# Kernel optimization log

Measured on AMD Instinct MI355X. Metric: run time of the kernel, lower is better.

## Reference

```python
import jax, jax.numpy as jnp
import numpy as np

B, L, R, D, K, H = 512, 10, 2048, 256, 20, 128
VOCAB, GEO_V, GEO_D = 30000, 1000, 64

def _l2norm(x):
    # F.normalize(p=2, dim=-1): x / max(||x||, eps)
    return x / jnp.maximum(jnp.linalg.norm(x, axis=-1, keepdims=True), 1e-12)

def setup_inputs() -> dict:
    key = jax.random.key(0)
    ks = jax.random.split(key, 20)
    emb = 0.02 * jax.random.normal(ks[0], (VOCAB, D), jnp.float32)
    emb = emb.at[0].set(0.0)  # padding_idx=0 row is zero
    inp = {
        'text_left': jax.random.randint(ks[1], (B, L), 0, VOCAB),
        'text_right': jax.random.randint(ks[2], (B, R), 0, VOCAB),
        'location_left': jax.random.randint(ks[3], (B, 2), 0, GEO_V),
        'distance': jax.random.uniform(ks[4], (B,), jnp.float32),
        'emb': emb,
        'attn_w': 0.05 * jax.random.normal(ks[5], (D,), jnp.float32),
        'w_m0': 0.1 * jax.random.normal(ks[6], (K, H), jnp.float32),
        'b_m0': jnp.zeros((H,), jnp.float32),
        'w_m1': 0.1 * jax.random.normal(ks[7], (H, H), jnp.float32),
        'b_m1': jnp.zeros((H,), jnp.float32),
        'w_m2': 0.1 * jax.random.normal(ks[8], (H, 1), jnp.float32),
        'b_m2': jnp.zeros((1,), jnp.float32),
        'out_w': 0.5 * jax.random.normal(ks[9], (1, 1), jnp.float32),
        'out_b': jnp.zeros((1,), jnp.float32),
        'lat_tab': 0.05 * jax.random.normal(ks[10], (GEO_V, GEO_D), jnp.float32),
        'lon_tab': 0.05 * jax.random.normal(ks[11], (GEO_V, GEO_D), jnp.float32),
        'w3': 0.05 * jax.random.normal(ks[12], (D, 10), jnp.float32),
        'b3': jnp.zeros((10,), jnp.float32),
        'w5': 0.05 * jax.random.normal(ks[13], (GEO_D, 32), jnp.float32),
        'b5': jnp.zeros((32,), jnp.float32),
        'w4': 0.05 * jax.random.normal(ks[14], (164, 2), jnp.float32),
        'b4': jnp.zeros((2,), jnp.float32),
    }
    return inp

def reference(text_left, text_right, location_left, distance, emb, attn_w,
              w_m0, b_m0, w_m1, b_m1, w_m2, b_m2, out_w, out_b,
              lat_tab, lon_tab, w3, b3, w5, b5, w4, b4):
    # ---- no_grad block in the original ----
    mask_query = text_left == 0  # mask_value = 0
    embed_query = emb[text_left]            # [B,L,D]
    embed_doc = emb[text_right]             # [B,R,D]
    matching = jnp.einsum('bld,brd->blr', _l2norm(embed_query), _l2norm(embed_doc))
    topk = jax.lax.top_k(matching, K)[0]    # [B,L,K], sorted descending
    logits = jnp.einsum('bld,d->bl', embed_query, attn_w)
    logits = jnp.where(mask_query, -jnp.inf, logits)
    attn = jax.nn.softmax(logits, axis=-1)  # [B,L]
    h = jnp.tanh(topk @ w_m0 + b_m0)
    h = jnp.tanh(h @ w_m1 + b_m1)
    h = jnp.tanh(h @ w_m2 + b_m2)[..., 0]   # [B,L]
    x = jnp.einsum('bl,bl->b', h, attn)[:, None]  # [B,1]
    x = jnp.tanh(x @ out_w + out_b)         # out layer (tanh)
    x = jax.lax.stop_gradient(x)
    embed_query = jax.lax.stop_gradient(embed_query)
    # ---- trainable geo/weighting branch ----
    lat = lat_tab[location_left[:, 0]] @ w5 + b5   # [B,32]
    lon = lon_tab[location_left[:, 1]] @ w5 + b5   # [B,32]
    q1 = (embed_query @ w3 + b3).reshape(embed_query.shape[0], -1)  # [B,100]
    w = jnp.concatenate([q1, lat, lon], axis=-1) @ w4 + b4          # [B,2]
    x_all = jnp.concatenate([x, distance[:, None]], axis=1)         # [B,2]
    pred = jnp.sum(w * x_all, axis=1, keepdims=True)                # [B,1]
    return pred
```

## Files before the change

### kernel.cpp

```cpp
#include <hip/hip_runtime.h>
#include <hip/hip_fp16.h>
#include <math.h>

#define BB 512
#define LL 10
#define RR 2048
#define DD 256
#define KK 20
#define HH 128
#define NVOCAB 30000
#define GEOD 64

#define FP4_SCALE   24.0f
#define FP4_DESCALE (1.0f / 576.0f)

#define EMB4_BYTES (NVOCAB * 128)
#define BLOB1_OFF  EMB4_BYTES
#define BLOB2_OFF  (BLOB1_OFF + 8192)
#define W3T_OFF    (BLOB2_OFF + 32768)
#define W5T_OFF    (W3T_OFF + 10240)

typedef __attribute__((ext_vector_type(2))) long long llx2;
typedef __attribute__((ext_vector_type(4))) float f32x4;
typedef __attribute__((ext_vector_type(8))) short bf16x8;
typedef __attribute__((ext_vector_type(8))) int   i32x8;

static __device__ inline unsigned short f2bf(float f) {
    unsigned u = __float_as_uint(f);
    unsigned r = (u + 0x7fff + ((u >> 16) & 1)) >> 16;
    return (unsigned short)r;
}

static __device__ inline unsigned q_e2m1(float x) {
    unsigned s = (x < 0.f) ? 8u : 0u;
    float a = fabsf(x);
    unsigned c = (a < 0.25f) ? 0u : (a < 0.75f) ? 1u : (a < 1.25f) ? 2u :
                 (a < 1.75f) ? 3u : (a < 2.5f)  ? 4u : (a < 3.5f)  ? 5u :
                 (a < 5.0f)  ? 6u : 7u;
    return s | c;
}

__global__ __launch_bounds__(256) void pre_kernel(
    const float* __restrict__ emb,
    const float* __restrict__ w_m0, const float* __restrict__ w_m1,
    const float* __restrict__ w3,   const float* __restrict__ w5,
    unsigned char* __restrict__ emb4,
    unsigned short* __restrict__ blob1, unsigned short* __restrict__ blob2,
    float* __restrict__ w3T, float* __restrict__ w5T)
{
    if (blockIdx.x < 7500) {
        int row  = blockIdx.x * 4 + (threadIdx.x >> 6);
        int lane = threadIdx.x & 63;
        float4 v = *(const float4*)(emb + (size_t)row * DD + lane * 4);
        float ssq = v.x * v.x + v.y * v.y + v.z * v.z + v.w * v.w;
        #pragma unroll
        for (int off = 32; off; off >>= 1) ssq += __shfl_xor(ssq, off);
        float s = FP4_SCALE / fmaxf(sqrtf(ssq), 1e-12f);
        unsigned n0 = q_e2m1(v.x * s), n1 = q_e2m1(v.y * s);
        unsigned n2 = q_e2m1(v.z * s), n3 = q_e2m1(v.w * s);
        unsigned short pk = (unsigned short)(n0 | (n1 << 4) | (n2 << 8) | (n3 << 12));
        ((unsigned short*)(emb4 + (size_t)row * 128))[lane] = pk;
    } else {
        int i = (blockIdx.x - 7500) * 256 + threadIdx.x;
        if (i < 4096) {
            int t = i >> 9, ln = (i >> 3) & 63, tt = i & 7;
            int n = t * 16 + (ln & 15), k = (ln >> 4) * 8 + tt;
            blob1[i] = (k < KK) ? f2bf(w_m0[k * HH + n]) : (unsigned short)0;
        } else if (i < 4096 + 16384) {
            int i2 = i - 4096;
            int ks = i2 >> 12, rem = i2 & 4095;
            int t = rem >> 9, ln = (rem >> 3) & 63, tt = rem & 7;
            int n = t * 16 + (ln & 15), k = ks * 32 + (ln >> 4) * 8 + tt;
            blob2[i2] = f2bf(w_m1[k * HH + n]);
        } else if (i < 4096 + 16384 + 2560) {
            int i3 = i - (4096 + 16384);
            int j = i3 >> 8, d = i3 & 255;
            w3T[i3] = w3[d * 10 + j];
        } else if (i < 4096 + 16384 + 2560 + 2048) {
            int i4 = i - (4096 + 16384 + 2560);
            int c = i4 >> 6, d = i4 & 63;
            w5T[i4] = w5[d * 32 + c];
        }
    }
}

static __device__ inline unsigned wave_umax_u32(unsigned x)
{
    unsigned t;
    t = (unsigned)__builtin_amdgcn_update_dpp((int)x, (int)x, 0x111, 0xF, 0xF, false); x = x > t ? x : t;
    t = (unsigned)__builtin_amdgcn_update_dpp((int)x, (int)x, 0x112, 0xF, 0xF, false); x = x > t ? x : t;
    t = (unsigned)__builtin_amdgcn_update_dpp((int)x, (int)x, 0x114, 0xF, 0xF, false); x = x > t ? x : t;
    t = (unsigned)__builtin_amdgcn_update_dpp((int)x, (int)x, 0x118, 0xF, 0xF, false); x = x > t ? x : t;
    t = (unsigned)__builtin_amdgcn_update_dpp((int)x, (int)x, 0x142, 0xF, 0xF, false); x = x > t ? x : t;
    t = (unsigned)__builtin_amdgcn_update_dpp((int)x, (int)x, 0x143, 0xF, 0xF, false); x = x > t ? x : t;
    return (unsigned)__builtin_amdgcn_readlane((int)x, 63);
}

static __device__ inline void build_top2(const unsigned short* __restrict__ row,
                                         int lane, unsigned extmask,
                                         unsigned& k1, unsigned& k2)
{
    unsigned m1 = 0u, m2 = 0u;
    #pragma unroll
    for (int k = 0; k < 32; ++k) {
        int j = lane + 64 * k;
        unsigned key = ((unsigned)row[j] << 16) | (unsigned)(2047 - j);
        key = ((extmask >> k) & 1u) ? 0u : key;
        unsigned mn = m1 < key ? m1 : key;
        m1 = m1 > key ? m1 : key;
        m2 = m2 > mn ? m2 : mn;
    }
    k1 = m1; k2 = m2;
}

__global__ __launch_bounds__(512, 4) void fused_kernel(
    const int*   __restrict__ text_left,
    const int*   __restrict__ text_right,
    const int*   __restrict__ loc_left,
    const float* __restrict__ distance,
    const float* __restrict__ emb,
    const float* __restrict__ attn_w,
    const float* __restrict__ b_m0, const float* __restrict__ b_m1,
    const float* __restrict__ w_m2, const float* __restrict__ b_m2,
    const float* __restrict__ out_w, const float* __restrict__ out_b,
    const float* __restrict__ lat_tab, const float* __restrict__ lon_tab,
    const float* __restrict__ b3, const float* __restrict__ b5,
    const float* __restrict__ w4, const float* __restrict__ b4,
    const unsigned char*  __restrict__ emb4,
    const unsigned short* __restrict__ blob1,
    const unsigned short* __restrict__ blob2,
    const float* __restrict__ w3T, const float* __restrict__ w5T,
    float*       __restrict__ out)
{
    __shared__ __align__(16) unsigned char arena[16384];
    __shared__ __align__(16) unsigned short s_keys[LL][RR];
    __shared__ __align__(8) unsigned short s_docs[RR];
    __shared__ float s_logit[LL];
    __shared__ float s_h[16];
    __shared__ float s_feat[164];

    unsigned short* s_h1   = (unsigned short*)arena;
    float*          s_topk = (float*)(arena + 4096);

    const int b    = blockIdx.x;
    const int tid  = threadIdx.x;
    const int lane = tid & 63;
    const int wid  = tid >> 6;
    const int m15  = lane & 15, q = lane >> 4;

    {
        unsigned* s_cnt = (unsigned*)arena;
        unsigned* s_off = (unsigned*)(arena + 1024);
        if (tid < 256) s_cnt[tid] = 0u;
        __syncthreads();
        const int* trb = text_right + b * RR;
        int dv[4];
        #pragma unroll
        for (int i = 0; i < 4; ++i) {
            dv[i] = trb[tid * 4 + i];
            atomicAdd(&s_cnt[dv[i] >> 7], 1u);
        }
        __syncthreads();
        if (tid < 256) s_off[tid + 1] = s_cnt[tid];
        if (tid == 0) s_off[0] = 0u;
        __syncthreads();
        #pragma unroll 1
        for (int st = 1; st < 256; st <<= 1) {
            unsigned v = 0u;
            if (tid < 256 && tid + 1 > st) v = s_off[tid + 1 - st];
            __syncthreads();
            if (tid < 256 && tid + 1 > st) s_off[tid + 1] += v;
            __syncthreads();
        }
        #pragma unroll
        for (int i = 0; i < 4; ++i) {
            unsigned p = atomicAdd(&s_off[dv[i] >> 7], 1u);
            s_docs[p] = (unsigned short)dv[i];
        }
        __syncthreads();
    }

    {
        i32x8 a0, a1;
        {
            int qidx = (m15 < LL) ? text_left[b * LL + m15] : 0;
            const unsigned char* ap = emb4 + (size_t)qidx * 128;
            uint4 f0 = *(const uint4*)(ap + q * 16);
            uint4 f1 = *(const uint4*)(ap + 64 + q * 16);
            a0 = (i32x8){(int)f0.x, (int)f0.y, (int)f0.z, (int)f0.w, 0, 0, 0, 0};
            a1 = (i32x8){(int)f1.x, (int)f1.y, (int)f1.z, (int)f1.w, 0, 0, 0, 0};
        }
        const int r0 = lane >> 3;
        const int c  = lane & 7;

        unsigned char* stg = arena + wid * 2048;

        int  I0, I1;
        llx2 R0, R1;

        auto LOADI = [&](int i) {
            int T = wid + 8 * i;
            I0 = (int)s_docs[T * 16 + r0];
            I1 = (int)s_docs[T * 16 + 8 + r0];
        };
        auto LOADR = [&]() {
            R0 = *(const llx2*)(emb4 + (size_t)I0 * 128 + (c << 4));
            R1 = *(const llx2*)(emb4 + (size_t)I1 * 128 + (c << 4));
        };
        auto STORE = [&]() {
            *(llx2*)(stg + r0 * 128 + ((c ^ r0) << 4))       = R0;
            *(llx2*)(stg + (8 + r0) * 128 + ((c ^ r0) << 4)) = R1;
        };
        auto COMPUTE = [&](int i) {
            uint4 b0 = *(const uint4*)(stg + m15 * 128 + ((q ^ (m15 & 7)) << 4));
            uint4 b1 = *(const uint4*)(stg + m15 * 128 + (((4 + q) ^ (m15 & 7)) << 4));
            i32x8 bb0 = {(int)b0.x, (int)b0.y, (int)b0.z, (int)b0.w, 0, 0, 0, 0};
            i32x8 bb1 = {(int)b1.x, (int)b1.y, (int)b1.z, (int)b1.w, 0, 0, 0, 0};
            f32x4 acc = {0.f, 0.f, 0.f, 0.f};
            acc = __builtin_amdgcn_mfma_scale_f32_16x16x128_f8f6f4(
                      a0, bb0, acc, 4, 4, 0, 0x7F7F7F7F, 0, 0x7F7F7F7F);
            acc = __builtin_amdgcn_mfma_scale_f32_16x16x128_f8f6f4(
                      a1, bb1, acc, 4, 4, 0, 0x7F7F7F7F, 0, 0x7F7F7F7F);
            int n0 = (wid + 8 * i) * 16;
            #pragma unroll
            for (int v = 0; v < 4; ++v) {
                int m = q * 4 + v;
                if (m < LL) {
                    float sc = acc[v] * FP4_DESCALE;
                    unsigned hb = (unsigned)__half_as_ushort(__float2half(sc));
                    unsigned ok = hb ^ ((hb & 0x8000u) ? 0xFFFFu : 0x8000u);
                    s_keys[m][n0 + m15] = (unsigned short)ok;
                }
            }
        };

        LOADI(0); LOADR(); LOADI(1);
        #pragma unroll 1
        for (int t = 0; t < 16; ++t) {
            STORE();
            if (t < 15) {
                LOADR();
                if (t < 14) LOADI(t + 2);
            }
            COMPUTE(t);
        }
    }
    __syncthreads();

    {
        int row = tid >> 5, col = tid & 31;
        if (row >= LL || col >= KK) s_topk[row * 32 + col] = 0.f;
    }

    {
        auto TOPK_ROW = [&](int l) {
            const unsigned short* krow = &s_keys[l][0];
            unsigned extmask = 0u, k1, k2;
            build_top2(krow, lane, extmask, k1, k2);
            #pragma unroll 1
            for (int it = 0; it < KK; ++it) {
                unsigned bmk = wave_umax_u32(k1);
                if (k1 == bmk) {
                    unsigned o16 = bmk >> 16;
                    unsigned hbv = (o16 & 0x8000u) ? (o16 & 0x7FFFu) : (o16 ^ 0xFFFFu);
                    s_topk[l * 32 + it] = __half2float(__ushort_as_half((unsigned short)hbv));
                    int j = 2047 - (int)(bmk & 0xFFFFu);
                    extmask |= 1u << (j >> 6);
                    k1 = k2; k2 = 0u;
                }
                if (__any(k1 == 0u)) {
                    if (k1 == 0u) build_top2(krow, lane, extmask, k1, k2);
                }
            }
        };
        TOPK_ROW(wid);
        if (wid >= 6) {
            TOPK_ROW(wid + 2);
        } else if (wid == 4) {
            const float4 aw = *(const float4*)(attn_w + lane * 4);
            for (int l = 0; l < LL; ++l) {
                int v = text_left[b * LL + l];
                float4 qv = *(const float4*)(emb + (size_t)v * DD + lane * 4);
                float d = qv.x * aw.x + qv.y * aw.y + qv.z * aw.z + qv.w * aw.w;
                #pragma unroll
                for (int off = 32; off; off >>= 1) d += __shfl_xor(d, off);
                if (lane == 0) s_logit[l] = (v == 0) ? -INFINITY : d;
            }
        } else if (wid == 5) {
            int c2 = lane & 31, which = lane >> 5;
            int v = loc_left[b * 2 + which];
            const float* tab = which ? lon_tab : lat_tab;
            const float4* tr = (const float4*)(tab + (size_t)v * GEOD);
            const float4* wr = (const float4*)(w5T + c2 * GEOD);
            float a = b5[c2];
            #pragma unroll
            for (int d4 = 0; d4 < 16; ++d4) {
                float4 tv = tr[d4], wv = wr[d4];
                a += tv.x * wv.x + tv.y * wv.y + tv.z * wv.z + tv.w * wv.w;
            }
            s_feat[100 + which * 32 + c2] = a;
        } else if (wid == 2 || wid == 3) {
            int p = (wid - 2) * 64 + lane;
            if (p < 100) {
                int l = p / 10, j = p % 10;
                int v = text_left[b * LL + l];
                const float4* qr = (const float4*)(emb + (size_t)v * DD);
                const float4* wr = (const float4*)(w3T + j * DD);
                float a = b3[j];
                #pragma unroll 8
                for (int d4 = 0; d4 < 64; ++d4) {
                    float4 qv = qr[d4], wv = wr[d4];
                    a += qv.x * wv.x + qv.y * wv.y + qv.z * wv.z + qv.w * wv.w;
                }
                s_feat[p] = a;
            }
        }
    }
    __syncthreads();

    if (wid == 0) {
        float tv[8];
        *(float4*)(tv)     = *(const float4*)(&s_topk[m15 * 32 + q * 8]);
        *(float4*)(tv + 4) = *(const float4*)(&s_topk[m15 * 32 + q * 8 + 4]);
        bf16x8 a1;
        #pragma unroll
        for (int t = 0; t < 8; ++t) a1[t] = (short)f2bf(tv[t]);
        f32x4 acc1[8];
        #pragma unroll
        for (int t = 0; t < 8; ++t) {
            bf16x8 b1 = *(const bf16x8*)(blob1 + t * 512 + lane * 8);
            f32x4 z = {0.f, 0.f, 0.f, 0.f};
            acc1[t] = __builtin_amdgcn_mfma_f32_16x16x32_bf16(a1, b1, z, 0, 0, 0);
        }
        #pragma unroll
        for (int t = 0; t < 8; ++t) {
            int c = t * 16 + m15;
            float bb0 = b_m0[c];
            #pragma unroll
            for (int v = 0; v < 4; ++v) {
                int m = q * 4 + v;
                float h = tanhf(acc1[t][v] + bb0);
                s_h1[m * 128 + (((c >> 3) ^ m) << 3) + (c & 7)] = f2bf(h);
            }
        }
        f32x4 acc2[8];
        #pragma unroll
        for (int t = 0; t < 8; ++t) acc2[t] = (f32x4){0.f, 0.f, 0.f, 0.f};
        #pragma unroll
        for (int ks = 0; ks < 4; ++ks) {
            bf16x8 a2 = *(const bf16x8*)(s_h1 + m15 * 128 + (((ks * 4 + q) ^ m15) << 3));
            #pragma unroll
            for (int t = 0; t < 8; ++t) {
                bf16x8 b2 = *(const bf16x8*)(blob2 + (ks * 8 + t) * 512 + lane * 8);
                acc2[t] = __builtin_amdgcn_mfma_f32_16x16x32_bf16(a2, b2, acc2[t], 0, 0, 0);
            }
        }
        float part[4] = {0.f, 0.f, 0.f, 0.f};
        #pragma unroll
        for (int t = 0; t < 8; ++t) {
            int c = t * 16 + m15;
            float bb1 = b_m1[c];
            float wm2 = w_m2[c];
            #pragma unroll
            for (int v = 0; v < 4; ++v)
                part[v] += tanhf(acc2[t][v] + bb1) * wm2;
        }
        #pragma unroll
        for (int v = 0; v < 4; ++v) {
            #pragma unroll
            for (int off = 1; off < 16; off <<= 1) part[v] += __shfl_xor(part[v], off);
        }
        if (m15 == 0) {
            #pragma unroll
            for (int v = 0; v < 4; ++v) {
                int m = q * 4 + v;
                if (m < LL) s_h[m] = tanhf(part[v] + b_m2[0]);
            }
        }
        float w0p = 0.f, w1p = 0.f;
        #pragma unroll
        for (int i = lane; i < 164; i += 64) {
            float f = s_feat[i];
            w0p += f * w4[i * 2 + 0];
            w1p += f * w4[i * 2 + 1];
        }
        #pragma unroll
        for (int off = 32; off; off >>= 1) {
            w0p += __shfl_xor(w0p, off);
            w1p += __shfl_xor(w1p, off);
        }
        if (lane == 0) {
            float mx = -INFINITY;
            #pragma unroll
            for (int l = 0; l < LL; ++l) mx = fmaxf(mx, s_logit[l]);
            float ex[LL];
            float sum = 0.f;
            #pragma unroll
            for (int l = 0; l < LL; ++l) { ex[l] = expf(s_logit[l] - mx); sum += ex[l]; }
            float x = 0.f;
            #pragma unroll
            for (int l = 0; l < LL; ++l) x += s_h[l] * (ex[l] / sum);
            float xo = tanhf(x * out_w[0] + out_b[0]);
            out[b] = (w0p + b4[0]) * xo + (w1p + b4[1]) * distance[b];
        }
    }
}

extern "C" void kernel_launch(void* const* d_in, const int* in_sizes, int n_in,
                              void* d_out, int out_size, void* d_ws, size_t ws_size,
                              hipStream_t stream) {
    const int*   text_left  = (const int*)  d_in[0];
    const int*   text_right = (const int*)  d_in[1];
    const int*   loc_left   = (const int*)  d_in[2];
    const float* distance   = (const float*)d_in[3];
    const float* emb        = (const float*)d_in[4];
    const float* attn_w     = (const float*)d_in[5];
    const float* w_m0       = (const float*)d_in[6];
    const float* b_m0       = (const float*)d_in[7];
    const float* w_m1       = (const float*)d_in[8];
    const float* b_m1       = (const float*)d_in[9];
    const float* w_m2       = (const float*)d_in[10];
    const float* b_m2       = (const float*)d_in[11];
    const float* out_w      = (const float*)d_in[12];
    const float* out_b      = (const float*)d_in[13];
    const float* lat_tab    = (const float*)d_in[14];
    const float* lon_tab    = (const float*)d_in[15];
    const float* w3         = (const float*)d_in[16];
    const float* b3         = (const float*)d_in[17];
    const float* w5         = (const float*)d_in[18];
    const float* b5         = (const float*)d_in[19];
    const float* w4         = (const float*)d_in[20];
    const float* b4         = (const float*)d_in[21];

    unsigned char*  ws    = (unsigned char*)d_ws;
    unsigned char*  emb4  = ws;
    unsigned short* blob1 = (unsigned short*)(ws + BLOB1_OFF);
    unsigned short* blob2 = (unsigned short*)(ws + BLOB2_OFF);
    float*          w3T   = (float*)(ws + W3T_OFF);
    float*          w5T   = (float*)(ws + W5T_OFF);
    float*          out   = (float*)d_out;

    pre_kernel<<<7598, 256, 0, stream>>>(emb, w_m0, w_m1, w3, w5,
                                         emb4, blob1, blob2, w3T, w5T);

    fused_kernel<<<BB, 512, 0, stream>>>(
        text_left, text_right, loc_left, distance, emb, attn_w,
        b_m0, b_m1, w_m2, b_m2, out_w, out_b,
        lat_tab, lon_tab, b3, b5, w4, b4,
        emb4, blob1, blob2, w3T, w5T, out);
}
```

Before: 51.02 us.

## Move doc-index bucket sort into pre-kernel and double-buffer staging tiles

The per-batch counting sort of text_right indices by vocab bucket moves out of the fused kernel into extra blocks of the pre-kernel, which write sorted indices to the workspace. The fused kernel then reads them from global memory, dropping several block-wide barriers and the shared s_docs array. The per-wave staging buffer doubles to two halves, alternated per tile iteration so a store does not overwrite data still being read. This costs an extra global write and read of the sorted indices and a larger shared arena, which may reduce occupancy.

```diff
diff --git a/kernel.cpp b/kernel.cpp
--- a/kernel.cpp
+++ b/kernel.cpp
@@ -19,6 +19,7 @@
 #define BLOB2_OFF  (BLOB1_OFF + 8192)
 #define W3T_OFF    (BLOB2_OFF + 32768)
 #define W5T_OFF    (W3T_OFF + 10240)
+#define SORT_OFF   (W5T_OFF + 8192)
 
 typedef __attribute__((ext_vector_type(2))) long long llx2;
 typedef __attribute__((ext_vector_type(4))) float f32x4;
@@ -44,10 +45,15 @@
     const float* __restrict__ emb,
     const float* __restrict__ w_m0, const float* __restrict__ w_m1,
     const float* __restrict__ w3,   const float* __restrict__ w5,
+    const int*   __restrict__ text_right,
     unsigned char* __restrict__ emb4,
     unsigned short* __restrict__ blob1, unsigned short* __restrict__ blob2,
-    float* __restrict__ w3T, float* __restrict__ w5T)
+    float* __restrict__ w3T, float* __restrict__ w5T,
+    unsigned short* __restrict__ sortd)
 {
+    __shared__ unsigned s_cnt[256];
+    __shared__ unsigned s_off[257];
+
     if (blockIdx.x < 7500) {
         int row  = blockIdx.x * 4 + (threadIdx.x >> 6);
         int lane = threadIdx.x & 63;
@@ -60,7 +66,7 @@
         unsigned n2 = q_e2m1(v.z * s), n3 = q_e2m1(v.w * s);
         unsigned short pk = (unsigned short)(n0 | (n1 << 4) | (n2 << 8) | (n3 << 12));
         ((unsigned short*)(emb4 + (size_t)row * 128))[lane] = pk;
-    } else {
+    } else if (blockIdx.x < 7598) {
         int i = (blockIdx.x - 7500) * 256 + threadIdx.x;
         if (i < 4096) {
             int t = i >> 9, ln = (i >> 3) & 63, tt = i & 7;
@@ -81,6 +87,36 @@
             int c = i4 >> 6, d = i4 & 63;
             w5T[i4] = w5[d * 32 + c];
         }
+    } else {
+        int b   = blockIdx.x - 7598;
+        int tid = threadIdx.x;
+        if (tid < 256) s_cnt[tid] = 0u;
+        __syncthreads();
+        const int* trb = text_right + b * RR;
+        int dv[8];
+        #pragma unroll
+        for (int i = 0; i < 8; ++i) {
+            dv[i] = trb[tid * 8 + i];
+            atomicAdd(&s_cnt[dv[i] >> 7], 1u);
+        }
+        __syncthreads();
+        if (tid < 256) s_off[tid + 1] = s_cnt[tid];
+        if (tid == 0) s_off[0] = 0u;
+        __syncthreads();
+        #pragma unroll 1
+        for (int st = 1; st < 256; st <<= 1) {
+            unsigned v = 0u;
+            if (tid < 256 && tid + 1 > st) v = s_off[tid + 1 - st];
+            __syncthreads();
+            if (tid < 256 && tid + 1 > st) s_off[tid + 1] += v;
+            __syncthreads();
+        }
+        unsigned short* dst = sortd + (size_t)b * RR;
+        #pragma unroll
+        for (int i = 0; i < 8; ++i) {
+            unsigned p = atomicAdd(&s_off[dv[i] >> 7], 1u);
+            dst[p] = (unsigned short)dv[i];
+        }
     }
 }
 
@@ -115,7 +151,6 @@
 
 __global__ __launch_bounds__(512, 4) void fused_kernel(
     const int*   __restrict__ text_left,
-    const int*   __restrict__ text_right,
     const int*   __restrict__ loc_left,
     const float* __restrict__ distance,
     const float* __restrict__ emb,
@@ -130,11 +165,11 @@
     const unsigned short* __restrict__ blob1,
     const unsigned short* __restrict__ blob2,
     const float* __restrict__ w3T, const float* __restrict__ w5T,
+    const unsigned short* __restrict__ sortd,
     float*       __restrict__ out)
 {
-    __shared__ __align__(16) unsigned char arena[16384];
+    __shared__ __align__(16) unsigned char arena[32768];
     __shared__ __align__(16) unsigned short s_keys[LL][RR];
-    __shared__ __align__(8) unsigned short s_docs[RR];
     __shared__ float s_logit[LL];
     __shared__ float s_h[16];
     __shared__ float s_feat[164];
@@ -147,38 +182,6 @@
     const int lane = tid & 63;
     const int wid  = tid >> 6;
     const int m15  = lane & 15, q = lane >> 4;
-
-    {
-        unsigned* s_cnt = (unsigned*)arena;
-        unsigned* s_off = (unsigned*)(arena + 1024);
-        if (tid < 256) s_cnt[tid] = 0u;
-        __syncthreads();
-        const int* trb = text_right + b * RR;
-        int dv[4];
-        #pragma unroll
-        for (int i = 0; i < 4; ++i) {
-            dv[i] = trb[tid * 4 + i];
-            atomicAdd(&s_cnt[dv[i] >> 7], 1u);
-        }
-        __syncthreads();
-        if (tid < 256) s_off[tid + 1] = s_cnt[tid];
-        if (tid == 0) s_off[0] = 0u;
-        __syncthreads();
-        #pragma unroll 1
-        for (int st = 1; st < 256; st <<= 1) {
-            unsigned v = 0u;
-            if (tid < 256 && tid + 1 > st) v = s_off[tid + 1 - st];
-            __syncthreads();
-            if (tid < 256 && tid + 1 > st) s_off[tid + 1] += v;
-            __syncthreads();
-        }
-        #pragma unroll
-        for (int i = 0; i < 4; ++i) {
-            unsigned p = atomicAdd(&s_off[dv[i] >> 7], 1u);
-            s_docs[p] = (unsigned short)dv[i];
-        }
-        __syncthreads();
-    }
 
     {
         i32x8 a0, a1;
@@ -193,27 +196,30 @@
         const int r0 = lane >> 3;
         const int c  = lane & 7;
 
-        unsigned char* stg = arena + wid * 2048;
+        const unsigned short* sb = sortd + (size_t)b * RR;
+        unsigned char* stg = arena + wid * 4096;
 
         int  I0, I1;
         llx2 R0, R1;
 
         auto LOADI = [&](int i) {
             int T = wid + 8 * i;
-            I0 = (int)s_docs[T * 16 + r0];
-            I1 = (int)s_docs[T * 16 + 8 + r0];
+            I0 = (int)sb[T * 16 + r0];
+            I1 = (int)sb[T * 16 + 8 + r0];
         };
         auto LOADR = [&]() {
             R0 = *(const llx2*)(emb4 + (size_t)I0 * 128 + (c << 4));
             R1 = *(const llx2*)(emb4 + (size_t)I1 * 128 + (c << 4));
         };
-        auto STORE = [&]() {
-            *(llx2*)(stg + r0 * 128 + ((c ^ r0) << 4))       = R0;
-            *(llx2*)(stg + (8 + r0) * 128 + ((c ^ r0) << 4)) = R1;
+        auto STORE = [&](int half) {
+            unsigned char* hb = stg + half * 2048;
+            *(llx2*)(hb + r0 * 128 + ((c ^ r0) << 4))       = R0;
+            *(llx2*)(hb + (8 + r0) * 128 + ((c ^ r0) << 4)) = R1;
         };
-        auto COMPUTE = [&](int i) {
-            uint4 b0 = *(const uint4*)(stg + m15 * 128 + ((q ^ (m15 & 7)) << 4));
-            uint4 b1 = *(const uint4*)(stg + m15 * 128 + (((4 + q) ^ (m15 & 7)) << 4));
+        auto COMPUTE = [&](int i, int half) {
+            const unsigned char* hb = stg + half * 2048;
+            uint4 b0 = *(const uint4*)(hb + m15 * 128 + ((q ^ (m15 & 7)) << 4));
+            uint4 b1 = *(const uint4*)(hb + m15 * 128 + (((4 + q) ^ (m15 & 7)) << 4));
             i32x8 bb0 = {(int)b0.x, (int)b0.y, (int)b0.z, (int)b0.w, 0, 0, 0, 0};
             i32x8 bb1 = {(int)b1.x, (int)b1.y, (int)b1.z, (int)b1.w, 0, 0, 0, 0};
             f32x4 acc = {0.f, 0.f, 0.f, 0.f};
@@ -227,8 +233,8 @@
                 int m = q * 4 + v;
                 if (m < LL) {
                     float sc = acc[v] * FP4_DESCALE;
-                    unsigned hb = (unsigned)__half_as_ushort(__float2half(sc));
-                    unsigned ok = hb ^ ((hb & 0x8000u) ? 0xFFFFu : 0x8000u);
+                    unsigned hbits = (unsigned)__half_as_ushort(__float2half(sc));
+                    unsigned ok = hbits ^ ((hbits & 0x8000u) ? 0xFFFFu : 0x8000u);
                     s_keys[m][n0 + m15] = (unsigned short)ok;
                 }
             }
@@ -237,12 +243,12 @@
         LOADI(0); LOADR(); LOADI(1);
         #pragma unroll 1
         for (int t = 0; t < 16; ++t) {
-            STORE();
+            STORE(t & 1);
             if (t < 15) {
                 LOADR();
                 if (t < 14) LOADI(t + 2);
             }
-            COMPUTE(t);
+            COMPUTE(t, t & 1);
         }
     }
     __syncthreads();
@@ -438,14 +444,15 @@
     unsigned short* blob2 = (unsigned short*)(ws + BLOB2_OFF);
     float*          w3T   = (float*)(ws + W3T_OFF);
     float*          w5T   = (float*)(ws + W5T_OFF);
+    unsigned short* sortd = (unsigned short*)(ws + SORT_OFF);
     float*          out   = (float*)d_out;
 
-    pre_kernel<<<7598, 256, 0, stream>>>(emb, w_m0, w_m1, w3, w5,
-                                         emb4, blob1, blob2, w3T, w5T);
+    pre_kernel<<<8110, 256, 0, stream>>>(emb, w_m0, w_m1, w3, w5, text_right,
+                                         emb4, blob1, blob2, w3T, w5T, sortd);
 
     fused_kernel<<<BB, 512, 0, stream>>>(
-        text_left, text_right, loc_left, distance, emb, attn_w,
+        text_left, loc_left, distance, emb, attn_w,
         b_m0, b_m1, w_m2, b_m2, out_w, out_b,
         lat_tab, lon_tab, b3, b5, w4, b4,
-        emb4, blob1, blob2, w3T, w5T, out);
-}
+        emb4, blob1, blob2, w3T, w5T, sortd, out);
+}
```

After: 53.20 us. 1.04x slower.
